# Kernel tuning notes

Hardware: AMD Instinct MI355X
Metric: run time of the kernel (lower is better)

The kernel has to match this reference:

```python
import jax, jax.numpy as jnp
import numpy as np

N = 50000      # nodes
E = 800000     # edges
F_IN = 128     # in_channels
H = 128        # hidden_channels
C = 10         # num_classes
G = 512        # graphs in batch
EPS = 1e-5     # batchnorm eps


def setup_inputs() -> dict:
    key = jax.random.key(0)
    ks = jax.random.split(key, 18)
    s = 0.05
    return {
        "x": jax.random.normal(ks[0], (N, F_IN), jnp.float32),
        "edge_index": jax.random.randint(ks[1], (2, E), 0, N, dtype=jnp.int32),
        "batch": jnp.sort(jax.random.randint(ks[2], (N,), 0, G, dtype=jnp.int32)),
        "W1": jax.random.normal(ks[3], (F_IN, H), jnp.float32) * s,
        "b1": jnp.zeros((H,), jnp.float32),
        "gamma1": jnp.ones((H,), jnp.float32),
        "beta1": jnp.zeros((H,), jnp.float32),
        "mean1": jax.random.normal(ks[4], (H,), jnp.float32) * 0.1,
        "var1": jax.random.uniform(ks[5], (H,), jnp.float32, 0.5, 1.5),
        "W2": jax.random.normal(ks[6], (H, H), jnp.float32) * s,
        "b2": jnp.zeros((H,), jnp.float32),
        "gamma2": jnp.ones((H,), jnp.float32),
        "beta2": jnp.zeros((H,), jnp.float32),
        "mean2": jax.random.normal(ks[7], (H,), jnp.float32) * 0.1,
        "var2": jax.random.uniform(ks[8], (H,), jnp.float32, 0.5, 1.5),
        "Wlin": jax.random.normal(ks[9], (H, C), jnp.float32) * s,
        "blin": jnp.zeros((C,), jnp.float32),
    }


def _gcn_conv(x, W, b, src, dst):
    # GCNConv with add_self_loops=True, symmetric normalization.
    h = x @ W                                             # [N, H]
    deg = jax.ops.segment_sum(jnp.ones((E,), h.dtype), dst, num_segments=N) + 1.0
    dis = jax.lax.rsqrt(deg)                              # deg^{-1/2}, [N]
    norm = dis[src] * dis[dst]                            # [E]
    agg = jax.ops.segment_sum(h[src] * norm[:, None], dst, num_segments=N)
    agg = agg + h * (dis * dis)[:, None]                  # self-loop term
    return agg + b


def _bn_eval(x, gamma, beta, mean, var):
    return gamma * (x - mean) * jax.lax.rsqrt(var + EPS) + beta


def reference(x, edge_index, batch, W1, b1, gamma1, beta1, mean1, var1,
              W2, b2, gamma2, beta2, mean2, var2, Wlin, blin):
    src, dst = edge_index[0], edge_index[1]
    h = _gcn_conv(x, W1, b1, src, dst)
    h = jax.nn.relu(_bn_eval(h, gamma1, beta1, mean1, var1))
    # dropout: identity in eval mode
    h = _gcn_conv(h, W2, b2, src, dst)
    h = jax.nn.relu(_bn_eval(h, gamma2, beta2, mean2, var2))
    # global_mean_pool over graph ids
    sums = jax.ops.segment_sum(h, batch, num_segments=G)          # [G, H]
    cnts = jax.ops.segment_sum(jnp.ones((N,), h.dtype), batch, num_segments=G)
    pooled = sums / jnp.maximum(cnts, 1.0)[:, None]
    return pooled @ Wlin + blin                                   # [G, C]
```

## Files before the change

### kernel.cpp

```cpp
#include <hip/hip_runtime.h>
#include <hip/hip_bf16.h>

#define N_NODES 50000
#define N_EDGES 800000
#define HDIM 128
#define NGRAPH 512
#define NCLS 10
#define BN_EPS 1e-5f
#define MAXDEG 64

typedef unsigned int  uint32;
typedef unsigned short ushort16;

__device__ inline float2 bf2f(uint32 u) {
    return make_float2(__uint_as_float(u << 16), __uint_as_float(u & 0xffff0000u));
}
__device__ inline ushort16 f2bf(float f) {
    uint32 u = __float_as_uint(f);
    u += 0x7fffu + ((u >> 16) & 1u);
    return (ushort16)(u >> 16);
}
__device__ inline uint32 packbf2(float lo, float hi) {
    return (uint32)f2bf(lo) | ((uint32)f2bf(hi) << 16);
}
__device__ inline float bfround(float f) {
    return __uint_as_float((uint32)f2bf(f) << 16);
}


#define GEMM1_BLOCKS 1563
#define FRONT_GRID (3 * GEMM1_BLOCKS)
#define AB_BLOCKS 1563

__global__ __launch_bounds__(256) void front(const float* __restrict__ x,
                                             const float* __restrict__ W1,
                                             ushort16* __restrict__ bufA,
                                             const int* __restrict__ src,
                                             const int* __restrict__ dst,
                                             int* __restrict__ deg,
                                             int* __restrict__ epad)
{
    __shared__ float xs[32][36];
    __shared__ float ws[32][128];
    const int tid = threadIdx.x;
    const int grp = blockIdx.x / 3, rem = blockIdx.x % 3;

    if (rem != 0) {
        int e = (grp * 2 + (rem - 1)) * 256 + tid;
        if (e < N_EDGES) {
            int d   = dst[e];
            int pos = atomicAdd(&deg[d], 1);
            epad[(size_t)d * MAXDEG + pos] = src[e];
        }
        return;
    }

    const int row0 = grp * 32;
    const int tx   = tid & 31;
    const int ty   = tid >> 5;

    float acc[4][4];
    #pragma unroll
    for (int i = 0; i < 4; ++i)
        #pragma unroll
        for (int j = 0; j < 4; ++j) acc[i][j] = 0.f;

    const int lr = tid >> 3;
    const int lk = (tid & 7) << 2;
    const int wr = tid >> 5;
    const int wc = (tid & 31) << 2;

    for (int k0 = 0; k0 < 128; k0 += 32) {
        float4 xv = make_float4(0.f, 0.f, 0.f, 0.f);
        int grow = row0 + lr;
        if (grow < N_NODES) xv = *(const float4*)(x + (size_t)grow * HDIM + k0 + lk);
        xs[lr][lk] = xv.x; xs[lr][lk + 1] = xv.y; xs[lr][lk + 2] = xv.z; xs[lr][lk + 3] = xv.w;
        #pragma unroll
        for (int i = 0; i < 4; ++i) {
            int kk = wr + i * 8;
            *(float4*)&ws[kk][wc] = *(const float4*)(W1 + (size_t)(k0 + kk) * HDIM + wc);
        }
        __syncthreads();
        #pragma unroll
        for (int kk = 0; kk < 32; kk += 4) {
            float4 wv[4];
            #pragma unroll
            for (int j = 0; j < 4; ++j) wv[j] = *(const float4*)&ws[kk + j][tx << 2];
            #pragma unroll
            for (int i = 0; i < 4; ++i) {
                float4 xr = *(const float4*)&xs[ty * 4 + i][kk];
                acc[i][0] += xr.x * wv[0].x; acc[i][1] += xr.x * wv[0].y;
                acc[i][2] += xr.x * wv[0].z; acc[i][3] += xr.x * wv[0].w;
                acc[i][0] += xr.y * wv[1].x; acc[i][1] += xr.y * wv[1].y;
                acc[i][2] += xr.y * wv[1].z; acc[i][3] += xr.y * wv[1].w;
                acc[i][0] += xr.z * wv[2].x; acc[i][1] += xr.z * wv[2].y;
                acc[i][2] += xr.z * wv[2].z; acc[i][3] += xr.z * wv[2].w;
                acc[i][0] += xr.w * wv[3].x; acc[i][1] += xr.w * wv[3].y;
                acc[i][2] += xr.w * wv[3].z; acc[i][3] += xr.w * wv[3].w;
            }
        }
        __syncthreads();
    }
    #pragma unroll
    for (int i = 0; i < 4; ++i) {
        int grow = row0 + ty * 4 + i;
        if (grow < N_NODES) {
            uint2 o;
            o.x = packbf2(acc[i][0], acc[i][1]);
            o.y = packbf2(acc[i][2], acc[i][3]);
            *(uint2*)(bufA + (size_t)grow * HDIM + (tx << 2)) = o;
        }
    }
}

__global__ __launch_bounds__(256) void rsqrt_deg(const int* __restrict__ deg_i,
                                                 float* __restrict__ dis, int n)
{
    int i = blockIdx.x * 256 + threadIdx.x;
    if (i < n) dis[i] = rsqrtf((float)deg_i[i] + 1.0f);
}

__device__ inline void gather_node_to_lds(const ushort16* __restrict__ h,
                                          const int* __restrict__ epad,
                                          const int* __restrict__ deg,
                                          const float* __restrict__ dis,
                                          const float* __restrict__ b,
                                          const float* __restrict__ gamma,
                                          const float* __restrict__ beta,
                                          const float* __restrict__ mean,
                                          const float* __restrict__ var,
                                          float (*hrow)[HDIM],
                                          int node, int r, int lane)
{
    const int q    = lane >> 4;
    const int ci   = (lane & 15) << 3;
    const int cnt_e = deg[node];
    const int base  = node * MAXDEG;
    const float dd  = dis[node];

    int   s_all  = 0;
    float nm_all = 0.f;
    if (lane < cnt_e) {
        s_all  = epad[base + lane];
        nm_all = dis[s_all] * dd;
    }

    float acc[8] = {0.f, 0.f, 0.f, 0.f, 0.f, 0.f, 0.f, 0.f};
    for (int j = q; j < cnt_e; j += 4) {
        int   s  = __shfl(s_all, j);
        float nm = __shfl(nm_all, j);
        uint4 v  = *(const uint4*)(h + (size_t)s * HDIM + ci);
        float2 f0 = bf2f(v.x), f1 = bf2f(v.y), f2 = bf2f(v.z), f3 = bf2f(v.w);
        acc[0] += f0.x * nm; acc[1] += f0.y * nm;
        acc[2] += f1.x * nm; acc[3] += f1.y * nm;
        acc[4] += f2.x * nm; acc[5] += f2.y * nm;
        acc[6] += f3.x * nm; acc[7] += f3.y * nm;
    }
    #pragma unroll
    for (int k = 0; k < 8; ++k) {
        acc[k] += __shfl_xor(acc[k], 16);
        acc[k] += __shfl_xor(acc[k], 32);
    }

    if (q == 0) {
        uint4 hv = *(const uint4*)(h + (size_t)node * HDIM + ci);
        float2 g0 = bf2f(hv.x), g1 = bf2f(hv.y), g2 = bf2f(hv.z), g3 = bf2f(hv.w);
        float a[8] = {acc[0] + g0.x * dd * dd, acc[1] + g0.y * dd * dd,
                      acc[2] + g1.x * dd * dd, acc[3] + g1.y * dd * dd,
                      acc[4] + g2.x * dd * dd, acc[5] + g2.y * dd * dd,
                      acc[6] + g3.x * dd * dd, acc[7] + g3.y * dd * dd};
        #pragma unroll
        for (int k = 0; k < 8; ++k) {
            int c = ci + k;
            float sc = gamma[c] * rsqrtf(var[c] + BN_EPS);
            float rr = (a[k] + b[c] - mean[c]) * sc + beta[c];
            hrow[r][c] = bfround(fmaxf(rr, 0.f));
        }
    }
}

__global__ __launch_bounds__(256) void gather1_gemm2(const ushort16* __restrict__ h,
                                                     const int* __restrict__ epad,
                                                     const int* __restrict__ deg,
                                                     const float* __restrict__ dis,
                                                     const float* __restrict__ b,
                                                     const float* __restrict__ gamma,
                                                     const float* __restrict__ beta,
                                                     const float* __restrict__ mean,
                                                     const float* __restrict__ var,
                                                     const float* __restrict__ W2,
                                                     ushort16* __restrict__ Y, int n)
{
    __shared__ float hrow[32][HDIM];
    __shared__ float ws[32][128];
    const int tid  = threadIdx.x;
    const int wave = tid >> 6, lane = tid & 63;
    const int node0 = blockIdx.x * 32;

    #pragma unroll 1
    for (int it = 0; it < 8; ++it) {
        int r = wave * 8 + it;
        int node = node0 + r;
        if (node < n)
            gather_node_to_lds(h, epad, deg, dis, b, gamma, beta, mean, var,
                               hrow, node, r, lane);
    }
    __syncthreads();

    const int tx = tid & 31;
    const int ty = tid >> 5;

    float acc[4][4];
    #pragma unroll
    for (int i = 0; i < 4; ++i)
        #pragma unroll
        for (int j = 0; j < 4; ++j) acc[i][j] = 0.f;

    const int wr = tid >> 5;
    const int wc = (tid & 31) << 2;

    for (int k0 = 0; k0 < 128; k0 += 32) {
        #pragma unroll
        for (int i = 0; i < 4; ++i) {
            int kk = wr + i * 8;
            *(float4*)&ws[kk][wc] = *(const float4*)(W2 + (size_t)(k0 + kk) * HDIM + wc);
        }
        __syncthreads();
        #pragma unroll
        for (int kk = 0; kk < 32; kk += 4) {
            float4 wv[4];
            #pragma unroll
            for (int j = 0; j < 4; ++j) wv[j] = *(const float4*)&ws[kk + j][tx << 2];
            #pragma unroll
            for (int i = 0; i < 4; ++i) {
                float4 xr = *(const float4*)&hrow[ty * 4 + i][k0 + kk];
                acc[i][0] += xr.x * wv[0].x; acc[i][1] += xr.x * wv[0].y;
                acc[i][2] += xr.x * wv[0].z; acc[i][3] += xr.x * wv[0].w;
                acc[i][0] += xr.y * wv[1].x; acc[i][1] += xr.y * wv[1].y;
                acc[i][2] += xr.y * wv[1].z; acc[i][3] += xr.y * wv[1].w;
                acc[i][0] += xr.z * wv[2].x; acc[i][1] += xr.z * wv[2].y;
                acc[i][2] += xr.z * wv[2].z; acc[i][3] += xr.z * wv[2].w;
                acc[i][0] += xr.w * wv[3].x; acc[i][1] += xr.w * wv[3].y;
                acc[i][2] += xr.w * wv[3].z; acc[i][3] += xr.w * wv[3].w;
            }
        }
        __syncthreads();
    }
    #pragma unroll
    for (int i = 0; i < 4; ++i) {
        int grow = node0 + ty * 4 + i;
        if (grow < n) {
            uint2 o;
            o.x = packbf2(acc[i][0], acc[i][1]);
            o.y = packbf2(acc[i][2], acc[i][3]);
            *(uint2*)(Y + (size_t)grow * HDIM + (tx << 2)) = o;
        }
    }
}

__global__ __launch_bounds__(256) void gather2_pool(const ushort16* __restrict__ h,
                                                    const int* __restrict__ epad,
                                                    const int* __restrict__ deg,
                                                    const float* __restrict__ dis,
                                                    const float* __restrict__ b,
                                                    const float* __restrict__ gamma,
                                                    const float* __restrict__ beta,
                                                    const float* __restrict__ mean,
                                                    const float* __restrict__ var,
                                                    const int* __restrict__ batch,
                                                    float* __restrict__ sums,
                                                    float* __restrict__ cnt, int n)
{
    __shared__ float hrow[32][HDIM];
    const int tid  = threadIdx.x;
    const int wave = tid >> 6, lane = tid & 63;
    const int node0 = blockIdx.x * 32;

    #pragma unroll 1
    for (int it = 0; it < 8; ++it) {
        int r = wave * 8 + it;
        int node = node0 + r;
        if (node < n)
            gather_node_to_lds(h, epad, deg, dis, b, gamma, beta, mean, var,
                               hrow, node, r, lane);
    }
    __syncthreads();

    if (tid < 128) {
        int c = tid;
        int nvalid = min(node0 + 32, n) - node0;
        int curg = batch[node0];
        float acc = 0.f;
        int run = 0;
        for (int i = 0; i < nvalid; ++i) {
            int g   = batch[node0 + i];
            float v = hrow[i][c];
            if (g != curg) {
                atomicAdd(&sums[(size_t)curg * HDIM + c], acc);
                if (c == 0) atomicAdd(&cnt[curg], (float)run);
                acc = 0.f; run = 0; curg = g;
            }
            acc += v; run++;
        }
        atomicAdd(&sums[(size_t)curg * HDIM + c], acc);
        if (c == 0) atomicAdd(&cnt[curg], (float)run);
    }
}

__global__ __launch_bounds__(128) void final_lin(const float* __restrict__ sums,
                                                 const float* __restrict__ cnt,
                                                 const float* __restrict__ Wlin,
                                                 const float* __restrict__ blin,
                                                 float* __restrict__ out)
{
    __shared__ float red[NCLS][2];
    int g = blockIdx.x;
    int t = threadIdx.x;
    float ic = 1.f / fmaxf(cnt[g], 1.f);
    float v  = sums[(size_t)g * HDIM + t] * ic;
    float p[NCLS];
    #pragma unroll
    for (int c = 0; c < NCLS; ++c) p[c] = v * Wlin[t * NCLS + c];
    #pragma unroll
    for (int c = 0; c < NCLS; ++c) {
        float x = p[c];
        for (int off = 32; off > 0; off >>= 1) x += __shfl_down(x, off);
        if ((t & 63) == 0) red[c][t >> 6] = x;
    }
    __syncthreads();
    if (t < NCLS) out[g * NCLS + t] = red[t][0] + red[t][1] + blin[t];
}

extern "C" void kernel_launch(void* const* d_in, const int* in_sizes, int n_in,
                              void* d_out, int out_size, void* d_ws, size_t ws_size,
                              hipStream_t stream)
{
    const float* x     = (const float*)d_in[0];
    const int*   ei    = (const int*)d_in[1];
    const int*   srcp  = ei;
    const int*   dstp  = ei + N_EDGES;
    const int*   batch = (const int*)d_in[2];
    const float* W1    = (const float*)d_in[3];
    const float* b1    = (const float*)d_in[4];
    const float* g1    = (const float*)d_in[5];
    const float* be1   = (const float*)d_in[6];
    const float* m1    = (const float*)d_in[7];
    const float* v1    = (const float*)d_in[8];
    const float* W2    = (const float*)d_in[9];
    const float* b2    = (const float*)d_in[10];
    const float* g2    = (const float*)d_in[11];
    const float* be2   = (const float*)d_in[12];
    const float* m2    = (const float*)d_in[13];
    const float* v2    = (const float*)d_in[14];
    const float* Wlin  = (const float*)d_in[15];
    const float* blin  = (const float*)d_in[16];
    float*       out   = (float*)d_out;

    ushort16* bufA = (ushort16*)d_ws;
    ushort16* bufB = bufA + (size_t)N_NODES * HDIM;
    int*   epad = (int*)(bufB + (size_t)N_NODES * HDIM);
    int*   deg  = epad + (size_t)N_NODES * MAXDEG;
    float* cnt  = (float*)(deg + N_NODES);
    float* sums = cnt + NGRAPH;
    float* dis  = sums + (size_t)NGRAPH * HDIM;

    hipMemsetAsync(deg, 0,
                   (N_NODES + NGRAPH + (size_t)NGRAPH * HDIM) * sizeof(float), stream);

    front<<<FRONT_GRID, 256, 0, stream>>>(x, W1, bufA, srcp, dstp, deg, epad);
    rsqrt_deg<<<(N_NODES + 255) / 256, 256, 0, stream>>>(deg, dis, N_NODES);

    gather1_gemm2<<<AB_BLOCKS, 256, 0, stream>>>(bufA, epad, deg, dis,
                                                 b1, g1, be1, m1, v1, W2, bufB, N_NODES);
    gather2_pool<<<AB_BLOCKS, 256, 0, stream>>>(bufB, epad, deg, dis,
                                                b2, g2, be2, m2, v2, batch,
                                                sums, cnt, N_NODES);
    final_lin<<<NGRAPH, 128, 0, stream>>>(sums, cnt, Wlin, blin, out);
}
```

Before: 283.3 us.

## Prefetch gather rows, store LDS tiles as bf16, fold zeroing into rsqrt kernel

The edge gather loop now issues the next neighbour row load before accumulating the current one, software-pipelining the random global reads. The per-block LDS staging buffers switch from fp32 to bf16, halving shared memory so more blocks can fit per CU; out-of-range rows are explicitly zeroed. The memset of the pool sums and counts moves into the rsqrt_deg kernel, which gets a larger grid, so the stream keeps a memset only for deg. The bf16 staging matches the rounding the code already did, so accuracy should be unchanged.

```diff
diff --git a/kernel.cpp b/kernel.cpp
--- a/kernel.cpp
+++ b/kernel.cpp
@@ -22,9 +22,6 @@
 }
 __device__ inline uint32 packbf2(float lo, float hi) {
     return (uint32)f2bf(lo) | ((uint32)f2bf(hi) << 16);
-}
-__device__ inline float bfround(float f) {
-    return __uint_as_float((uint32)f2bf(f) << 16);
 }
 
 
@@ -113,11 +110,14 @@
     }
 }
 
+#define CZ_DWORDS (NGRAPH + NGRAPH * HDIM)
 __global__ __launch_bounds__(256) void rsqrt_deg(const int* __restrict__ deg_i,
-                                                 float* __restrict__ dis, int n)
+                                                 float* __restrict__ dis,
+                                                 uint32* __restrict__ cz, int n)
 {
     int i = blockIdx.x * 256 + threadIdx.x;
     if (i < n) dis[i] = rsqrtf((float)deg_i[i] + 1.0f);
+    if (i < CZ_DWORDS) cz[i] = 0;
 }
 
 __device__ inline void gather_node_to_lds(const ushort16* __restrict__ h,
@@ -129,7 +129,7 @@
                                           const float* __restrict__ beta,
                                           const float* __restrict__ mean,
                                           const float* __restrict__ var,
-                                          float (*hrow)[HDIM],
+                                          ushort16 (*hrow)[HDIM],
                                           int node, int r, int lane)
 {
     const int q    = lane >> 4;
@@ -146,15 +146,25 @@
     }
 
     float acc[8] = {0.f, 0.f, 0.f, 0.f, 0.f, 0.f, 0.f, 0.f};
-    for (int j = q; j < cnt_e; j += 4) {
-        int   s  = __shfl(s_all, j);
-        float nm = __shfl(nm_all, j);
-        uint4 v  = *(const uint4*)(h + (size_t)s * HDIM + ci);
-        float2 f0 = bf2f(v.x), f1 = bf2f(v.y), f2 = bf2f(v.z), f3 = bf2f(v.w);
-        acc[0] += f0.x * nm; acc[1] += f0.y * nm;
-        acc[2] += f1.x * nm; acc[3] += f1.y * nm;
-        acc[4] += f2.x * nm; acc[5] += f2.y * nm;
-        acc[6] += f3.x * nm; acc[7] += f3.y * nm;
+    int j = q;
+    int   s_cur  = __shfl(s_all, j);
+    float nm_cur = __shfl(nm_all, j);
+    uint4 v_cur  = make_uint4(0, 0, 0, 0);
+    if (j < cnt_e)
+        v_cur = *(const uint4*)(h + (size_t)s_cur * HDIM + ci);
+    while (j < cnt_e) {
+        const int jn = j + 4;
+        int   s_nxt  = __shfl(s_all, jn & 63);
+        float nm_nxt = __shfl(nm_all, jn & 63);
+        uint4 v_nxt  = make_uint4(0, 0, 0, 0);
+        if (jn < cnt_e)
+            v_nxt = *(const uint4*)(h + (size_t)s_nxt * HDIM + ci);
+        float2 f0 = bf2f(v_cur.x), f1 = bf2f(v_cur.y), f2 = bf2f(v_cur.z), f3 = bf2f(v_cur.w);
+        acc[0] += f0.x * nm_cur; acc[1] += f0.y * nm_cur;
+        acc[2] += f1.x * nm_cur; acc[3] += f1.y * nm_cur;
+        acc[4] += f2.x * nm_cur; acc[5] += f2.y * nm_cur;
+        acc[6] += f3.x * nm_cur; acc[7] += f3.y * nm_cur;
+        v_cur = v_nxt; nm_cur = nm_nxt; j = jn;
     }
     #pragma unroll
     for (int k = 0; k < 8; ++k) {
@@ -174,7 +184,7 @@
             int c = ci + k;
             float sc = gamma[c] * rsqrtf(var[c] + BN_EPS);
             float rr = (a[k] + b[c] - mean[c]) * sc + beta[c];
-            hrow[r][c] = bfround(fmaxf(rr, 0.f));
+            hrow[r][c] = f2bf(fmaxf(rr, 0.f));
         }
     }
 }
@@ -191,7 +201,7 @@
                                                      const float* __restrict__ W2,
                                                      ushort16* __restrict__ Y, int n)
 {
-    __shared__ float hrow[32][HDIM];
+    __shared__ ushort16 hrow[32][HDIM];
     __shared__ float ws[32][128];
     const int tid  = threadIdx.x;
     const int wave = tid >> 6, lane = tid & 63;
@@ -204,6 +214,11 @@
         if (node < n)
             gather_node_to_lds(h, epad, deg, dis, b, gamma, beta, mean, var,
                                hrow, node, r, lane);
+        else if ((lane >> 4) == 0) {
+            int ci = (lane & 15) << 3;
+            #pragma unroll
+            for (int k = 0; k < 8; ++k) hrow[r][ci + k] = 0;
+        }
     }
     __syncthreads();
 
@@ -233,7 +248,9 @@
             for (int j = 0; j < 4; ++j) wv[j] = *(const float4*)&ws[kk + j][tx << 2];
             #pragma unroll
             for (int i = 0; i < 4; ++i) {
-                float4 xr = *(const float4*)&hrow[ty * 4 + i][k0 + kk];
+                uint2 u = *(const uint2*)&hrow[ty * 4 + i][k0 + kk];
+                float2 xa = bf2f(u.x), xb = bf2f(u.y);
+                float4 xr = make_float4(xa.x, xa.y, xb.x, xb.y);
                 acc[i][0] += xr.x * wv[0].x; acc[i][1] += xr.x * wv[0].y;
                 acc[i][2] += xr.x * wv[0].z; acc[i][3] += xr.x * wv[0].w;
                 acc[i][0] += xr.y * wv[1].x; acc[i][1] += xr.y * wv[1].y;
@@ -271,7 +288,7 @@
                                                     float* __restrict__ sums,
                                                     float* __restrict__ cnt, int n)
 {
-    __shared__ float hrow[32][HDIM];
+    __shared__ ushort16 hrow[32][HDIM];
     const int tid  = threadIdx.x;
     const int wave = tid >> 6, lane = tid & 63;
     const int node0 = blockIdx.x * 32;
@@ -294,7 +311,7 @@
         int run = 0;
         for (int i = 0; i < nvalid; ++i) {
             int g   = batch[node0 + i];
-            float v = hrow[i][c];
+            float v = __uint_as_float((uint32)hrow[i][c] << 16);
             if (g != curg) {
                 atomicAdd(&sums[(size_t)curg * HDIM + c], acc);
                 if (c == 0) atomicAdd(&cnt[curg], (float)run);
@@ -364,11 +381,10 @@
     float* sums = cnt + NGRAPH;
     float* dis  = sums + (size_t)NGRAPH * HDIM;
 
-    hipMemsetAsync(deg, 0,
-                   (N_NODES + NGRAPH + (size_t)NGRAPH * HDIM) * sizeof(float), stream);
+    hipMemsetAsync(deg, 0, N_NODES * sizeof(int), stream);
 
     front<<<FRONT_GRID, 256, 0, stream>>>(x, W1, bufA, srcp, dstp, deg, epad);
-    rsqrt_deg<<<(N_NODES + 255) / 256, 256, 0, stream>>>(deg, dis, N_NODES);
+    rsqrt_deg<<<(CZ_DWORDS + 255) / 256, 256, 0, stream>>>(deg, dis, (uint32*)cnt, N_NODES);
 
     gather1_gemm2<<<AB_BLOCKS, 256, 0, stream>>>(bufA, epad, deg, dis,
                                                  b1, g1, be1, m1, v1, W2, bufB, N_NODES);
```

New measurement: 279.5 us. About the same (-1.3%).
